# Performance work log

Hardware: AMD Instinct MI355X
Metric: run time of the kernel (lower is better)

The kernel has to match this reference:

```python
import jax, jax.numpy as jnp
import numpy as np

E = 1024      # embedding_size
K = 64        # key_size
D = 64        # head_size
S = 1024      # context_size
V = 32000     # vocab_size
H = 16        # layer_size (heads per layer)
L = 8         # num_layers
B = 2


def _pe():
    pos = jnp.arange(S, dtype=jnp.float32)[:, None]
    i = jnp.arange(E, dtype=jnp.float32)[None, :]
    ang = pos / jnp.power(10000.0, 2.0 * i / E)
    return jnp.where((jnp.arange(E) % 2 == 0)[None, :], jnp.sin(ang), jnp.cos(ang))


def setup_inputs() -> dict:
    key = jax.random.key(0)
    ks = iter(jax.random.split(key, 32))
    s = 0.02
    n = lambda shape: jax.random.normal(next(ks), shape, dtype=jnp.float32) * s
    inp = {
        "tokens": jax.random.randint(next(ks), (B, S), 0, V),
        "emb": n((V, E)),
        "pe": _pe(),
        "k1w": n((L, H, K, E)), "k1b": n((L, H, K)),
        "k2w": n((L, H, K, K)), "k2b": n((L, H, K)),
        "q1w": n((L, H, K, E)), "q1b": n((L, H, K)),
        "q2w": n((L, H, K, K)), "q2b": n((L, H, K)),
        "vw": n((L, H, D, E)), "vb": n((L, H, D)),
        "lnw": jnp.ones((L, E), jnp.float32), "lnb": jnp.zeros((L, E), jnp.float32),
        "p1w": n((L, E, E)), "p1b": n((L, E)),
        "p2w": n((L, E, E)), "p2b": n((L, E)),
        "predw": n((V, E)), "predb": n((V,)),
    }
    return inp


def reference(tokens, emb, pe, k1w, k1b, k2w, k2b, q1w, q1b, q2w, q2b,
              vw, vb, lnw, lnb, p1w, p1b, p2w, p2b, predw, predb):
    relu = jax.nn.relu
    x = emb[tokens] + pe[:tokens.shape[1]]                       # [B,S,E]
    seq = tokens.shape[1]
    # Faithful to original: tril (past+diag) gets the -1e10 penalty.
    mask = jnp.tril(jnp.ones((seq, seq), x.dtype)) * -1e10
    for l in range(L):
        # two-layer ReLU MLPs for K and Q, batched over heads
        k = relu(jnp.einsum('bse,hke->bhsk', x, k1w[l]) + k1b[l][None, :, None, :])
        k = relu(jnp.einsum('bhsk,hjk->bhsj', k, k2w[l]) + k2b[l][None, :, None, :])
        q = relu(jnp.einsum('bse,hke->bhsk', x, q1w[l]) + q1b[l][None, :, None, :])
        q = relu(jnp.einsum('bhsk,hjk->bhsj', q, q2w[l]) + q2b[l][None, :, None, :])
        v = jnp.einsum('bse,hde->bhsd', x, vw[l]) + vb[l][None, :, None, :]
        scores = jnp.einsum('bhsk,bhtk->bhst', q, k) / (K ** 0.5) + mask
        w = jax.nn.softmax(scores, axis=-1)
        o = jnp.einsum('bhst,bhtd->bhsd', w, v)                  # [B,H,S,D]
        o = o.transpose(0, 2, 1, 3).reshape(x.shape[0], seq, H * D)
        y = x + o
        mu = y.mean(-1, keepdims=True)
        var = ((y - mu) ** 2).mean(-1, keepdims=True)
        yn = (y - mu) / jnp.sqrt(var + 1e-5) * lnw[l] + lnb[l]
        h1 = relu(yn @ p1w[l].T + p1b[l])
        x = relu(h1 @ p2w[l].T + p2b[l])
    logits = x @ predw.T + predb                                 # [B,S,V]
    return logits
```

## Files before the change

kernel.cpp:

```cpp
#include <hip/hip_runtime.h>


typedef __attribute__((ext_vector_type(8))) short bf16x8;
typedef __attribute__((ext_vector_type(4))) float f32x4;

#define L_ 8
#define S_ 1024
#define E_ 1024
#define B_ 2
#define H_ 16
#define V_ 32000
#define M_ 2048

__device__ __forceinline__ unsigned short f2b(float f) {
  union { float f; unsigned int u; } v; v.f = f;
  unsigned int r = v.u + 0x7FFFu + ((v.u >> 16) & 1u);
  return (unsigned short)(r >> 16);
}

#define GLDS16(gptr, lptr)                                                            \
  __builtin_amdgcn_global_load_lds(                                                   \
      (const __attribute__((address_space(1))) unsigned int*)(gptr),                  \
      (__attribute__((address_space(3))) unsigned int*)(lptr), 16, 0, 0)

__global__ void cvt_kernel(const float* __restrict__ src, unsigned short* __restrict__ dst) {
  size_t i = ((size_t)blockIdx.x * 256 + threadIdx.x) * 4;
  float4 v = *(const float4*)(src + i);
  unsigned short* d = dst + i;
  d[0] = f2b(v.x); d[1] = f2b(v.y); d[2] = f2b(v.z); d[3] = f2b(v.w);
}

__global__ void cvt_seg_kernel(const float* __restrict__ src, unsigned short* __restrict__ dst,
                               int perLayer, int dstStride, int dstOff) {
  size_t i = ((size_t)blockIdx.x * 256 + threadIdx.x) * 4;
  int l = (int)(i / perLayer);
  int off = (int)(i - (size_t)l * perLayer);
  float4 v = *(const float4*)(src + i);
  unsigned short* d = dst + (size_t)l * dstStride + dstOff + off;
  d[0] = f2b(v.x); d[1] = f2b(v.y); d[2] = f2b(v.z); d[3] = f2b(v.w);
}

__global__ void biascat_kernel(const float* __restrict__ k1b, const float* __restrict__ q1b,
                               const float* __restrict__ vb, float* __restrict__ bcat) {
  int i = blockIdx.x * 256 + threadIdx.x;
  int l = i / 3072, j = i - l * 3072;
  float v;
  if (j < 1024)      v = k1b[l * 1024 + j];
  else if (j < 2048) v = q1b[l * 1024 + j - 1024];
  else               v = vb [l * 1024 + j - 2048];
  bcat[i] = v;
}

__global__ void embed_kernel(const int* __restrict__ tokens, const float* __restrict__ emb,
                             const float* __restrict__ pe, float* __restrict__ x32,
                             unsigned short* __restrict__ xb) {
  int row = blockIdx.x;
  int s = row & (S_ - 1);
  int e0 = threadIdx.x * 4;
  int tok = tokens[row];
  float4 ev = *(const float4*)(emb + (size_t)tok * E_ + e0);
  float4 pv = *(const float4*)(pe + (size_t)s * E_ + e0);
  float4 v; v.x = ev.x + pv.x; v.y = ev.y + pv.y; v.z = ev.z + pv.z; v.w = ev.w + pv.w;
  *(float4*)(x32 + (size_t)row * E_ + e0) = v;
  ushort4 o; o.x = f2b(v.x); o.y = f2b(v.y); o.z = f2b(v.z); o.w = f2b(v.w);
  *(ushort4*)(xb + (size_t)row * E_ + e0) = o;
}

template <int BM, int BN, int RELU, int OBF, int OF32, int VT>
__global__ __launch_bounds__(256) void gemm97(
    const unsigned short* __restrict__ A, const unsigned short* __restrict__ W,
    const float* __restrict__ bias, unsigned short* __restrict__ Cb,
    float* __restrict__ Cf, unsigned short* __restrict__ vTp,
    int K, int N, int reluN) {
  constexpr int AR = BM / 64;
  constexpr int BR = BN / 64;
  constexpr int FM = BM / 32;
  constexpr int FN = BN / 32;
  __shared__ __align__(16) unsigned short sA[BM * 32];
  __shared__ __align__(16) unsigned short sB[BN * 32];
  const int tid = threadIdx.x;
  const int lane = tid & 63, wave = tid >> 6;
  const int l16 = lane & 15, lhi = lane >> 4;

  const int gx = gridDim.x, nwg = gx * gridDim.y;
  int o = blockIdx.y * gx + blockIdx.x;
  int wg = ((nwg & 7) == 0) ? ((o & 7) * (nwg >> 3) + (o >> 3)) : o;
  const int row0 = (wg % gx) * BM, col0 = (wg / gx) * BN;

  const int wm = (wave >> 1) * (BM / 2), wn = (wave & 1) * (BN / 2);

  const int srow = wave * 16 + (lane >> 2);
  const int scol = (lane & 3) * 8;

  f32x4 acc[FM][FN] = {};

  for (int k0 = 0; k0 < K; k0 += 32) {
#pragma unroll
    for (int r = 0; r < AR; r++)
      GLDS16(A + (size_t)(row0 + r * 64 + srow) * K + k0 + scol,
             sA + r * 2048 + wave * 512);
#pragma unroll
    for (int r = 0; r < BR; r++)
      GLDS16(W + (size_t)(col0 + r * 64 + srow) * K + k0 + scol,
             sB + r * 2048 + wave * 512);
    __syncthreads();

    bf16x8 af[FM], bf[FN];
#pragma unroll
    for (int i = 0; i < FM; i++)
      af[i] = *(const bf16x8*)(sA + (wm + i * 16 + l16) * 32 + lhi * 8);
#pragma unroll
    for (int j = 0; j < FN; j++)
      bf[j] = *(const bf16x8*)(sB + (wn + j * 16 + l16) * 32 + lhi * 8);
#pragma unroll
    for (int i = 0; i < FM; i++)
#pragma unroll
      for (int j = 0; j < FN; j++)
        acc[i][j] = __builtin_amdgcn_mfma_f32_16x16x32_bf16(bf[j], af[i], acc[i][j], 0, 0, 0);
    __syncthreads();
  }

#pragma unroll
  for (int j = 0; j < FN; j++) {
    const int colb = col0 + wn + j * 16 + lhi * 4;
    const float4 bv = *(const float4*)(bias + colb);
    const bool dorelu = (RELU == 1) || (RELU == 2 && colb < reluN);
#pragma unroll
    for (int i = 0; i < FM; i++) {
      const int row = row0 + wm + i * 16 + l16;
      float v0 = acc[i][j][0] + bv.x, v1 = acc[i][j][1] + bv.y;
      float v2 = acc[i][j][2] + bv.z, v3 = acc[i][j][3] + bv.w;
      if (dorelu) {
        v0 = fmaxf(v0, 0.f); v1 = fmaxf(v1, 0.f);
        v2 = fmaxf(v2, 0.f); v3 = fmaxf(v3, 0.f);
      }
      if (OBF) {
        ushort4 ob; ob.x = f2b(v0); ob.y = f2b(v1); ob.z = f2b(v2); ob.w = f2b(v3);
        *(ushort4*)(Cb + (size_t)row * N + colb) = ob;
      }
      if (OF32) {
        float4 of; of.x = v0; of.y = v1; of.z = v2; of.w = v3;
        *(float4*)(Cf + (size_t)row * N + colb) = of;
      }
      if (VT) {
        if (colb - lhi * 4 >= 2048) {
          const int hd0 = colb - 2048;
          const int bq = row >> 10, s = row & 1023;
          unsigned short* vr = vTp + ((size_t)(bq << 10) + hd0) * 1024 + s;
          vr[0] = f2b(v0); vr[1024] = f2b(v1); vr[2048] = f2b(v2); vr[3072] = f2b(v3);
        }
      }
    }
  }
}

__global__ __launch_bounds__(256) void k2q2_kernel(
    const unsigned short* __restrict__ kqv, const unsigned short* __restrict__ wk2,
    const unsigned short* __restrict__ wq2, const float* __restrict__ k2b,
    const float* __restrict__ q2b, unsigned short* __restrict__ kbuf,
    unsigned short* __restrict__ qbuf) {
  const int m0 = blockIdx.x * 64;
  const int h = blockIdx.y;
  const int which = blockIdx.z;
  const unsigned short* Ap = kqv + (which ? 1024 : 0) + h * 64;
  const unsigned short* Wp = (which ? wq2 : wk2) + h * 4096;
  const float* bias = (which ? q2b : k2b) + h * 64;
  unsigned short* out = (which ? qbuf : kbuf) + h * 64;
  const int lane = threadIdx.x & 63, wave = threadIdx.x >> 6;
  const int l16 = lane & 15, lhi = lane >> 4;
  const int mw = m0 + wave * 16;

  f32x4 acc[4] = {};
#pragma unroll
  for (int ks = 0; ks < 2; ks++) {
    bf16x8 a = *(const bf16x8*)(Ap + (size_t)(mw + l16) * 3072 + ks * 32 + (lhi << 3));
#pragma unroll
    for (int j = 0; j < 4; j++) {
      bf16x8 b = *(const bf16x8*)(Wp + (j * 16 + l16) * 64 + ks * 32 + (lhi << 3));
      acc[j] = __builtin_amdgcn_mfma_f32_16x16x32_bf16(a, b, acc[j], 0, 0, 0);
    }
  }
#pragma unroll
  for (int j = 0; j < 4; j++) {
    float bv = bias[j * 16 + l16];
#pragma unroll
    for (int r = 0; r < 4; r++) {
      int row = mw + (lhi << 2) + r;
      float v = fmaxf(acc[j][r] + bv, 0.f);
      out[(size_t)row * 1024 + j * 16 + l16] = f2b(v);
    }
  }
}

__global__ __launch_bounds__(128) void attn_kernel(
    const unsigned short* __restrict__ qbuf,
    const unsigned short* __restrict__ kbuf,
    const unsigned short* __restrict__ vT,
    float* __restrict__ o32) {
  constexpr int LD = 72;
  __shared__ __align__(16) unsigned short sP[2 * 16 * LD];
  const int bid = blockIdx.x;
  const int bh = bid & 31, qt = bid >> 5;
  const int b = bh >> 4, h = bh & 15;
  const int tid = threadIdx.x, lane = tid & 63, w = tid >> 6;
  const int l16 = lane & 15, lhi = lane >> 4;
  const int base = b * S_;
  const int qrow = qt * 32 + w * 16 + l16;

  bf16x8 aq[2];
#pragma unroll
  for (int ks = 0; ks < 2; ks++)
    aq[ks] = *(const bf16x8*)(qbuf + (size_t)(base + qrow) * 1024 + h * 64 + ks * 32 + (lhi << 3));

  f32x4 oacc[4] = {};
  float mrun[4], lrun[4];
#pragma unroll
  for (int r = 0; r < 4; r++) { mrun[r] = -1e10f; lrun[r] = 0.f; }
  const int srow = qt * 32 + w * 16 + (lhi << 2);
  const int t0s = (qt == 31) ? 0 : ((qt >> 1) << 6);

  unsigned short* sPw = sP + w * 16 * LD;

  for (int t0 = t0s; t0 < S_; t0 += 64) {
    f32x4 sacc[4] = {};
#pragma unroll
    for (int ks = 0; ks < 2; ks++) {
#pragma unroll
      for (int nt = 0; nt < 4; nt++) {
        bf16x8 bk = *(const bf16x8*)(kbuf + (size_t)(base + t0 + nt * 16 + l16) * 1024 +
                                     h * 64 + ks * 32 + (lhi << 3));
        sacc[nt] = __builtin_amdgcn_mfma_f32_16x16x32_bf16(aq[ks], bk, sacc[nt], 0, 0, 0);
      }
    }
    float p[4][4];
#pragma unroll
    for (int nt = 0; nt < 4; nt++) {
      int tcol = t0 + nt * 16 + l16;
#pragma unroll
      for (int r = 0; r < 4; r++) {
        float v = sacc[nt][r] * 0.125f;
        if (tcol <= srow + r) v = -1e10f;
        p[nt][r] = v;
      }
    }
#pragma unroll
    for (int r = 0; r < 4; r++) {
      float m = fmaxf(fmaxf(p[0][r], p[1][r]), fmaxf(p[2][r], p[3][r]));
#pragma unroll
      for (int off = 1; off < 16; off <<= 1) m = fmaxf(m, __shfl_xor(m, off, 16));
      float mnew = fmaxf(mrun[r], m);
      float alpha = __expf(mrun[r] - mnew);
      mrun[r] = mnew;
      float rs = 0.f;
#pragma unroll
      for (int nt = 0; nt < 4; nt++) {
        float e = __expf(p[nt][r] - mnew);
        p[nt][r] = e; rs += e;
      }
#pragma unroll
      for (int off = 1; off < 16; off <<= 1) rs += __shfl_xor(rs, off, 16);
      lrun[r] = lrun[r] * alpha + rs;
      oacc[0][r] *= alpha; oacc[1][r] *= alpha; oacc[2][r] *= alpha; oacc[3][r] *= alpha;
    }
#pragma unroll
    for (int nt = 0; nt < 4; nt++)
#pragma unroll
      for (int r = 0; r < 4; r++)
        sPw[((lhi << 2) + r) * LD + nt * 16 + l16] = f2b(p[nt][r]);
#pragma unroll
    for (int ks = 0; ks < 2; ks++) {
      bf16x8 ap = *(const bf16x8*)(sPw + l16 * LD + ks * 32 + (lhi << 3));
#pragma unroll
      for (int nt = 0; nt < 4; nt++) {
        bf16x8 bv = *(const bf16x8*)(vT + (size_t)(bh * 64 + nt * 16 + l16) * 1024 +
                                     t0 + ks * 32 + (lhi << 3));
        oacc[nt] = __builtin_amdgcn_mfma_f32_16x16x32_bf16(ap, bv, oacc[nt], 0, 0, 0);
      }
    }
  }
#pragma unroll
  for (int nt = 0; nt < 4; nt++) {
#pragma unroll
    for (int r = 0; r < 4; r++) {
      int row = srow + r;
      o32[(size_t)(base + row) * 1024 + h * 64 + nt * 16 + l16] = oacc[nt][r] / lrun[r];
    }
  }
}

__global__ __launch_bounds__(256) void ln_kernel(
    const float* __restrict__ x32, const float* __restrict__ o32,
    const float* __restrict__ lnw, const float* __restrict__ lnb,
    unsigned short* __restrict__ yn) {
  __shared__ float red[8];
  const int row = blockIdx.x, tid = threadIdx.x;
  const int lane = tid & 63, wave = tid >> 6;
  const int e0 = tid * 4;
  float4 xv = *(const float4*)(x32 + (size_t)row * E_ + e0);
  float4 ov = *(const float4*)(o32 + (size_t)row * E_ + e0);
  float y0 = xv.x + ov.x, y1 = xv.y + ov.y, y2 = xv.z + ov.z, y3 = xv.w + ov.w;
  float s = y0 + y1 + y2 + y3;
  float sq = y0 * y0 + y1 * y1 + y2 * y2 + y3 * y3;
#pragma unroll
  for (int off = 32; off > 0; off >>= 1) {
    s += __shfl_xor(s, off, 64);
    sq += __shfl_xor(sq, off, 64);
  }
  if (lane == 0) { red[wave * 2] = s; red[wave * 2 + 1] = sq; }
  __syncthreads();
  float ts = red[0] + red[2] + red[4] + red[6];
  float tsq = red[1] + red[3] + red[5] + red[7];
  float mu = ts * (1.f / E_);
  float var = tsq * (1.f / E_) - mu * mu;
  float rstd = rsqrtf(var + 1e-5f);
  float4 gv = *(const float4*)(lnw + e0);
  float4 bv = *(const float4*)(lnb + e0);
  ushort4 o;
  o.x = f2b((y0 - mu) * rstd * gv.x + bv.x);
  o.y = f2b((y1 - mu) * rstd * gv.y + bv.y);
  o.z = f2b((y2 - mu) * rstd * gv.z + bv.z);
  o.w = f2b((y3 - mu) * rstd * gv.w + bv.w);
  *(ushort4*)(yn + (size_t)row * E_ + e0) = o;
}

extern "C" void kernel_launch(void* const* d_in, const int* in_sizes, int n_in,
                              void* d_out, int out_size, void* d_ws, size_t ws_size,
                              hipStream_t stream) {
  const int* tokens  = (const int*)d_in[0];
  const float* emb   = (const float*)d_in[1];
  const float* pe    = (const float*)d_in[2];
  const float* k1w   = (const float*)d_in[3];
  const float* k1b   = (const float*)d_in[4];
  const float* k2w   = (const float*)d_in[5];
  const float* k2b   = (const float*)d_in[6];
  const float* q1w   = (const float*)d_in[7];
  const float* q1b   = (const float*)d_in[8];
  const float* q2w   = (const float*)d_in[9];
  const float* q2b   = (const float*)d_in[10];
  const float* vw    = (const float*)d_in[11];
  const float* vb    = (const float*)d_in[12];
  const float* lnw   = (const float*)d_in[13];
  const float* lnb   = (const float*)d_in[14];
  const float* p1w   = (const float*)d_in[15];
  const float* p1b   = (const float*)d_in[16];
  const float* p2w   = (const float*)d_in[17];
  const float* p2b   = (const float*)d_in[18];
  const float* predw = (const float*)d_in[19];
  const float* predb = (const float*)d_in[20];
  float* out = (float*)d_out;

  char* p = (char*)d_ws;
  auto alloc = [&](size_t bytes) -> char* {
    char* r = p; p += (bytes + 255) & ~(size_t)255; return r;
  };
  unsigned short* wcat  = (unsigned short*)alloc((size_t)L_ * 3072 * 1024 * 2);
  unsigned short* wk2   = (unsigned short*)alloc((size_t)L_ * H_ * 64 * 64 * 2);
  unsigned short* wq2   = (unsigned short*)alloc((size_t)L_ * H_ * 64 * 64 * 2);
  unsigned short* wp1   = (unsigned short*)alloc((size_t)L_ * 1024 * 1024 * 2);
  unsigned short* wp2   = (unsigned short*)alloc((size_t)L_ * 1024 * 1024 * 2);
  unsigned short* wpred = (unsigned short*)alloc((size_t)V_ * 1024 * 2);
  float*          bcat  = (float*)alloc((size_t)L_ * 3072 * 4);
  float*          x32   = (float*)alloc((size_t)M_ * 1024 * 4);
  unsigned short* xb    = (unsigned short*)alloc((size_t)M_ * 1024 * 2);
  unsigned short* kqv   = (unsigned short*)alloc((size_t)M_ * 3072 * 2);
  unsigned short* kbuf  = (unsigned short*)alloc((size_t)M_ * 1024 * 2);
  unsigned short* qbuf  = (unsigned short*)alloc((size_t)M_ * 1024 * 2);
  unsigned short* vTb   = (unsigned short*)alloc((size_t)32 * 64 * 1024 * 2);
  float*          o32   = (float*)alloc((size_t)M_ * 1024 * 4);
  unsigned short* yn    = (unsigned short*)alloc((size_t)M_ * 1024 * 2);
  unsigned short* h1    = (unsigned short*)alloc((size_t)M_ * 1024 * 2);
  if ((size_t)(p - (char*)d_ws) > ws_size) return;

  cvt_seg_kernel<<<8192, 256, 0, stream>>>(k1w, wcat, 1048576, 3145728, 0);
  cvt_seg_kernel<<<8192, 256, 0, stream>>>(q1w, wcat, 1048576, 3145728, 1048576);
  cvt_seg_kernel<<<8192, 256, 0, stream>>>(vw,  wcat, 1048576, 3145728, 2097152);
  cvt_kernel<<<512, 256, 0, stream>>>(k2w, wk2);
  cvt_kernel<<<512, 256, 0, stream>>>(q2w, wq2);
  cvt_kernel<<<8192, 256, 0, stream>>>(p1w, wp1);
  cvt_kernel<<<8192, 256, 0, stream>>>(p2w, wp2);
  cvt_kernel<<<32000, 256, 0, stream>>>(predw, wpred);
  biascat_kernel<<<96, 256, 0, stream>>>(k1b, q1b, vb, bcat);

  embed_kernel<<<M_, 256, 0, stream>>>(tokens, emb, pe, x32, xb);

  for (int l = 0; l < L_; l++) {
    const unsigned short* wcat_l = wcat + (size_t)l * 3072 * 1024;
    const float* bcat_l = bcat + (size_t)l * 3072;
    const unsigned short* wk2_l = wk2 + (size_t)l * H_ * 64 * 64;
    const unsigned short* wq2_l = wq2 + (size_t)l * H_ * 64 * 64;
    const unsigned short* wp1_l = wp1 + (size_t)l * 1024 * 1024;
    const unsigned short* wp2_l = wp2 + (size_t)l * 1024 * 1024;

    gemm97<128, 128, 2, 1, 0, 1><<<dim3(16, 24), 256, 0, stream>>>(
        xb, wcat_l, bcat_l, kqv, nullptr, vTb, 1024, 3072, 2048);
    k2q2_kernel<<<dim3(32, 16, 2), 256, 0, stream>>>(
        kqv, wk2_l, wq2_l, k2b + l * 1024, q2b + l * 1024, kbuf, qbuf);
    attn_kernel<<<1024, 128, 0, stream>>>(qbuf, kbuf, vTb, o32);
    ln_kernel<<<M_, 256, 0, stream>>>(x32, o32, lnw + l * 1024, lnb + l * 1024, yn);
    gemm97<64, 64, 1, 1, 0, 0><<<dim3(32, 16), 256, 0, stream>>>(
        yn, wp1_l, p1b + l * 1024, h1, nullptr, nullptr, 1024, 1024, 0);
    gemm97<64, 64, 1, 1, 1, 0><<<dim3(32, 16), 256, 0, stream>>>(
        h1, wp2_l, p2b + l * 1024, xb, x32, nullptr, 1024, 1024, 0);
  }

  gemm97<128, 128, 0, 0, 1, 0><<<dim3(16, 250), 256, 0, stream>>>(
      xb, wpred, predb, nullptr, out, nullptr, 1024, V_, 0);
}
```

Baseline: 1.496 ms.

## Add 256x256-tile GEMM for vocab projection and retile MLP GEMMs

Adds a dedicated 512-thread GEMM kernel for the final 2048x32000x1024 logits projection. It uses 256x256 output tiles, double-buffered direct-to-LDS loads, raised wave priority around the MFMA blocks, and an XCD-aware block remap. The larger tile is meant to raise arithmetic intensity and cut redundant weight traffic on the largest GEMM. The per-layer MLP GEMMs also change from 64x64 to 64x128 tiles, which halves their block count in exchange for more reuse per block.

Result: slower. 1.561 ms (+4.3%).

```diff
diff --git a/kernel.cpp b/kernel.cpp
--- a/kernel.cpp
+++ b/kernel.cpp
@@ -150,6 +150,120 @@
           vr[0] = f2b(v0); vr[1024] = f2b(v1); vr[2048] = f2b(v2); vr[3072] = f2b(v3);
         }
       }
+    }
+  }
+}
+
+__global__ __launch_bounds__(512, 2) void gemm256(
+    const unsigned short* __restrict__ A, const unsigned short* __restrict__ W,
+    const float* __restrict__ bias, float* __restrict__ Cf) {
+  constexpr int KK = 1024;
+  constexpr int NT = 32;
+  __shared__ __align__(16) unsigned short sA[2][8192];
+  __shared__ __align__(16) unsigned short sB[2][8192];
+  const int tid = threadIdx.x;
+  const int lane = tid & 63, wave = tid >> 6;
+  const int l16 = lane & 15, lhi = lane >> 4;
+  const int wr = wave >> 2, wc = wave & 3;
+
+  const int o = blockIdx.x;
+  const int wg = (o & 7) * 125 + (o >> 3);
+  const int row0 = (wg & 7) * 256;
+  const int col0 = (wg >> 3) * 256;
+
+  const int sr = tid >> 2, sc = (tid & 3) * 8;
+
+  f32x4 acc[8][4] = {};
+
+  auto stage = [&](int t) {
+    const int buf = t & 1;
+    const int k0 = t * 32;
+#pragma unroll
+    for (int is = 0; is < 2; is++) {
+      GLDS16(A + (size_t)(row0 + is * 128 + sr) * KK + k0 + sc,
+             &sA[buf][(is * 512 + (tid & ~63)) * 8]);
+      GLDS16(W + (size_t)(col0 + is * 128 + sr) * KK + k0 + sc,
+             &sB[buf][(is * 512 + (tid & ~63)) * 8]);
+    }
+  };
+
+  stage(0);
+  stage(1);
+
+  bf16x8 af[4], bf[4];
+  for (int t = 0; t < NT - 1; t++) {
+    const int buf = t & 1;
+    asm volatile("s_waitcnt vmcnt(4)" ::: "memory");
+    __builtin_amdgcn_s_barrier();
+    __builtin_amdgcn_sched_barrier(0);
+#pragma unroll
+    for (int j = 0; j < 4; j++)
+      bf[j] = *(const bf16x8*)(&sB[buf][(wc * 64 + j * 16 + l16) * 32 + lhi * 8]);
+#pragma unroll
+    for (int i = 0; i < 4; i++)
+      af[i] = *(const bf16x8*)(&sA[buf][(wr * 128 + i * 16 + l16) * 32 + lhi * 8]);
+    __builtin_amdgcn_s_setprio(1);
+#pragma unroll
+    for (int i = 0; i < 4; i++)
+#pragma unroll
+      for (int j = 0; j < 4; j++)
+        acc[i][j] = __builtin_amdgcn_mfma_f32_16x16x32_bf16(bf[j], af[i], acc[i][j], 0, 0, 0);
+    __builtin_amdgcn_s_setprio(0);
+#pragma unroll
+    for (int i = 0; i < 4; i++)
+      af[i] = *(const bf16x8*)(&sA[buf][(wr * 128 + 64 + i * 16 + l16) * 32 + lhi * 8]);
+    __builtin_amdgcn_s_setprio(1);
+#pragma unroll
+    for (int i = 0; i < 4; i++)
+#pragma unroll
+      for (int j = 0; j < 4; j++)
+        acc[i + 4][j] = __builtin_amdgcn_mfma_f32_16x16x32_bf16(bf[j], af[i], acc[i + 4][j], 0, 0, 0);
+    __builtin_amdgcn_s_setprio(0);
+    __builtin_amdgcn_s_barrier();
+    __builtin_amdgcn_sched_barrier(0);
+    if (t <= NT - 3) stage(t + 2);
+  }
+  {
+    const int buf = (NT - 1) & 1;
+    asm volatile("s_waitcnt vmcnt(0)" ::: "memory");
+    __builtin_amdgcn_s_barrier();
+    __builtin_amdgcn_sched_barrier(0);
+#pragma unroll
+    for (int j = 0; j < 4; j++)
+      bf[j] = *(const bf16x8*)(&sB[buf][(wc * 64 + j * 16 + l16) * 32 + lhi * 8]);
+#pragma unroll
+    for (int i = 0; i < 4; i++)
+      af[i] = *(const bf16x8*)(&sA[buf][(wr * 128 + i * 16 + l16) * 32 + lhi * 8]);
+    __builtin_amdgcn_s_setprio(1);
+#pragma unroll
+    for (int i = 0; i < 4; i++)
+#pragma unroll
+      for (int j = 0; j < 4; j++)
+        acc[i][j] = __builtin_amdgcn_mfma_f32_16x16x32_bf16(bf[j], af[i], acc[i][j], 0, 0, 0);
+    __builtin_amdgcn_s_setprio(0);
+#pragma unroll
+    for (int i = 0; i < 4; i++)
+      af[i] = *(const bf16x8*)(&sA[buf][(wr * 128 + 64 + i * 16 + l16) * 32 + lhi * 8]);
+    __builtin_amdgcn_s_setprio(1);
+#pragma unroll
+    for (int i = 0; i < 4; i++)
+#pragma unroll
+      for (int j = 0; j < 4; j++)
+        acc[i + 4][j] = __builtin_amdgcn_mfma_f32_16x16x32_bf16(bf[j], af[i], acc[i + 4][j], 0, 0, 0);
+    __builtin_amdgcn_s_setprio(0);
+  }
+
+#pragma unroll
+  for (int j = 0; j < 4; j++) {
+    const int colb = col0 + wc * 64 + j * 16 + lhi * 4;
+    const float4 bv = *(const float4*)(bias + colb);
+#pragma unroll
+    for (int i = 0; i < 8; i++) {
+      const int row = row0 + wr * 128 + i * 16 + l16;
+      float4 of;
+      of.x = acc[i][j][0] + bv.x; of.y = acc[i][j][1] + bv.y;
+      of.z = acc[i][j][2] + bv.z; of.w = acc[i][j][3] + bv.w;
+      *(float4*)(Cf + (size_t)row * V_ + colb) = of;
     }
   }
 }
@@ -397,12 +511,11 @@
         kqv, wk2_l, wq2_l, k2b + l * 1024, q2b + l * 1024, kbuf, qbuf);
     attn_kernel<<<1024, 128, 0, stream>>>(qbuf, kbuf, vTb, o32);
     ln_kernel<<<M_, 256, 0, stream>>>(x32, o32, lnw + l * 1024, lnb + l * 1024, yn);
-    gemm97<64, 64, 1, 1, 0, 0><<<dim3(32, 16), 256, 0, stream>>>(
+    gemm97<64, 128, 1, 1, 0, 0><<<dim3(32, 8), 256, 0, stream>>>(
         yn, wp1_l, p1b + l * 1024, h1, nullptr, nullptr, 1024, 1024, 0);
-    gemm97<64, 64, 1, 1, 1, 0><<<dim3(32, 16), 256, 0, stream>>>(
+    gemm97<64, 128, 1, 1, 1, 0><<<dim3(32, 8), 256, 0, stream>>>(
         h1, wp2_l, p2b + l * 1024, xb, x32, nullptr, 1024, 1024, 0);
   }
 
-  gemm97<128, 128, 0, 0, 1, 0><<<dim3(16, 250), 256, 0, stream>>>(
-      xb, wpred, predb, nullptr, out, nullptr, 1024, V_, 0);
-}
+  gemm256<<<1000, 512, 0, stream>>>(xb, wpred, predb, out);
+}
```
